# Kernel tuning notes

Measured on AMD Instinct MI355X. Metric: run time of the kernel, lower is better.

## Reference

```python
import jax, jax.numpy as jnp
import numpy as np

B, S, D = 2, 2048, 2048
NH, NKV, HD = 16, 4, 128
REP = NH // NKV
EPS = 1e-6
ROPE_THETA = 1e6


def setup_inputs() -> dict:
    key = jax.random.key(0)
    ks = jax.random.split(key, 6)
    x = jax.random.normal(ks[0], (B, S, D), jnp.float32)
    # real rotary embeddings: [S, HD]
    inv_freq = 1.0 / (ROPE_THETA ** (np.arange(0, HD, 2, dtype=np.float64) / HD))
    freqs = np.outer(np.arange(S, dtype=np.float64), inv_freq)
    emb = np.concatenate([freqs, freqs], axis=-1)
    cos = jnp.asarray(np.cos(emb), jnp.float32)
    sin = jnp.asarray(np.sin(emb), jnp.float32)
    scale = 1.0 / np.sqrt(D)
    Wq = jax.random.normal(ks[1], (D, NH * HD), jnp.float32) * scale   # [in, out]
    Wk = jax.random.normal(ks[2], (D, NKV * HD), jnp.float32) * scale
    Wv = jax.random.normal(ks[3], (D, NKV * HD), jnp.float32) * scale
    Wo = jax.random.normal(ks[4], (NH * HD, D), jnp.float32) * (1.0 / np.sqrt(NH * HD))
    q_norm_w = jnp.ones((HD,), jnp.float32)
    k_norm_w = jnp.ones((HD,), jnp.float32)
    return dict(x=x, cos=cos, sin=sin, Wq=Wq, Wk=Wk, Wv=Wv, Wo=Wo,
                q_norm_w=q_norm_w, k_norm_w=k_norm_w)


def _rms_norm(h, w):
    var = jnp.mean(h * h, axis=-1, keepdims=True)
    return w * (h * jax.lax.rsqrt(var + EPS))


def _rotate_half(h):
    h1, h2 = jnp.split(h, 2, axis=-1)
    return jnp.concatenate([-h2, h1], axis=-1)


def reference(x, cos, sin, Wq, Wk, Wv, Wo, q_norm_w, k_norm_w):
    b, s, _ = x.shape
    q = (x @ Wq).reshape(b, s, NH, HD)
    k = (x @ Wk).reshape(b, s, NKV, HD)
    v = (x @ Wv).reshape(b, s, NKV, HD)
    # per-head QK RMSNorm
    q = _rms_norm(q, q_norm_w)
    k = _rms_norm(k, k_norm_w)
    # RoPE: cos/sin [S,HD] -> broadcast over batch and heads
    c = cos[None, :, None, :]
    s_ = sin[None, :, None, :]
    q = q * c + _rotate_half(q) * s_
    k = k * c + _rotate_half(k) * s_
    # GQA: group q heads per kv head instead of materializing repeat_kv
    qg = q.reshape(b, s, NKV, REP, HD)
    scores = jnp.einsum('bqgrd,bkgd->bgrqk', qg, k) / np.sqrt(HD)
    causal = jnp.tril(jnp.ones((s, s), bool))  # [q,k]
    scores = jnp.where(causal, scores, -jnp.inf)
    probs = jax.nn.softmax(scores.astype(jnp.float32), axis=-1).astype(q.dtype)
    out = jnp.einsum('bgrqk,bkgd->bqgrd', probs, v).reshape(b, s, NH * HD)
    return out @ Wo
```

## Files before the change

kernel.cpp:

```cpp
#include <hip/hip_runtime.h>
#include <hip/hip_bf16.h>
#include <math.h>

#define B_ 2
#define S_ 2048
#define D_ 2048
#define NH_ 16
#define NKV_ 4
#define HD_ 128
#define EPS_ 1e-6f
#define SCALE_ 0.08838834764831845f
#define LOG2E_ 1.4426950408889634f
#define KOFF_ 2048
#define VOFF_ 2560
#define MINIT_ -1e30f

typedef float f32x4 __attribute__((ext_vector_type(4)));
typedef short bf16x8 __attribute__((ext_vector_type(8)));
typedef short short4v __attribute__((ext_vector_type(4)));
typedef float float4v __attribute__((ext_vector_type(4)));
typedef unsigned uint2v __attribute__((ext_vector_type(2)));
typedef unsigned uint4v __attribute__((ext_vector_type(4)));

static __device__ __forceinline__ short f2bf(float f) {
    union { float f; unsigned u; } x{f};
    unsigned r = (x.u + 0x7fff + ((x.u >> 16) & 1)) >> 16;
    return (short)r;
}
static __device__ __forceinline__ float bf2f(short s) {
    union { unsigned u; float f; } x; x.u = ((unsigned)(unsigned short)s) << 16; return x.f;
}
static __device__ __forceinline__ unsigned pack_bf2(float a, float b) {
    return __builtin_amdgcn_perm(__builtin_bit_cast(unsigned, b),
                                 __builtin_bit_cast(unsigned, a), 0x07060302u);
}

#define AS1(p) ((const __attribute__((address_space(1))) void*)(p))
#define AS3(p) ((__attribute__((address_space(3))) void*)(p))
static __device__ __forceinline__ void async16(const void* g, void* l) {
    __builtin_amdgcn_global_load_lds(AS1(g), AS3(l), 16, 0, 0);
}

__global__ __launch_bounds__(256) void cast_kernel(const float* __restrict__ in,
                                                   short* __restrict__ out) {
    size_t i = ((size_t)blockIdx.x * 256 + threadIdx.x) * 4;
    float4v v = *(const float4v*)(in + i);
    short4v o; o.x = f2bf(v.x); o.y = f2bf(v.y); o.z = f2bf(v.z); o.w = f2bf(v.w);
    *(short4v*)(out + i) = o;
}

__global__ __launch_bounds__(256) void transpose_all_kernel(const float* __restrict__ Wq,
                                                            const float* __restrict__ Wk,
                                                            const float* __restrict__ Wv,
                                                            const float* __restrict__ Wo,
                                                            short* __restrict__ Wt,
                                                            short* __restrict__ Wot) {
    __shared__ float tile[64][65];
    const int bx = blockIdx.x, by = blockIdx.y;
    const float* src; short* dst; int N, nb;
    if (bx < 32)      { src = Wq; dst = Wt;                         N = 2048; nb = bx; }
    else if (bx < 40) { src = Wk; dst = Wt + (size_t)KOFF_ * 2048;  N = 512;  nb = bx - 32; }
    else if (bx < 48) { src = Wv; dst = Wt + (size_t)VOFF_ * 2048;  N = 512;  nb = bx - 40; }
    else              { src = Wo; dst = Wot;                        N = 2048; nb = bx - 48; }
    const int n0 = nb * 64, k0 = by * 64;
    const int tid = threadIdx.x;
    for (int r = 0; r < 16; ++r) {
        int k = r * 4 + (tid >> 6);
        int n = tid & 63;
        tile[k][n] = src[(size_t)(k0 + k) * N + n0 + n];
    }
    __syncthreads();
    for (int r = 0; r < 4; ++r) {
        int n  = r * 16 + (tid >> 4);
        int kk = (tid & 15) * 4;
        short4v o4;
        o4.x = f2bf(tile[kk + 0][n]); o4.y = f2bf(tile[kk + 1][n]);
        o4.z = f2bf(tile[kk + 2][n]); o4.w = f2bf(tile[kk + 3][n]);
        *(short4v*)&dst[(size_t)(n0 + n) * 2048 + k0 + kk] = o4;
    }
}

__global__ __launch_bounds__(512, 2) void gemm_oproj_kernel(const short* __restrict__ A,
                                                            const short* __restrict__ Bt,
                                                            float* __restrict__ C) {
    __shared__ __align__(16) short smem[49152];
    short* A0 = smem;
    short* A1 = smem + 8192;
    short* B0 = smem + 16384;
    short* B1 = smem + 32768;

    const int tid  = threadIdx.x;
    const int orig = blockIdx.y * 8 + blockIdx.x;
    const int swz  = (orig & 7) * 32 + (orig >> 3);
    const int bn = swz & 7, bm = swz >> 3;
    const int wave = tid >> 6, lane = tid & 63;
    const int quad = lane >> 4, l16 = lane & 15;
    const int wr = wave >> 2, wc = wave & 3;

    const short* Ag = A  + (size_t)(bm * 128) * 2048;
    const short* Bg = Bt + (size_t)(bn * 256) * 2048;

    f32x4 acc[4][4];
#pragma unroll
    for (int i = 0; i < 4; ++i)
#pragma unroll
        for (int j = 0; j < 4; ++j) acc[i][j] = (f32x4){0.f, 0.f, 0.f, 0.f};

    bf16x8 a[4][2], b0[2][2], b1[2][2];

    auto stage_half = [&](const short* gpanel, int t, int h, short* lslot) {
#pragma unroll
        for (int u = 0; u < 2; ++u) {
            int ci = u * 512 + tid;
            int r  = ci >> 3;
            int cb = ((ci & 7) * 16) ^ ((r & 7) << 4);
            async16(gpanel + (size_t)(h * 128 + r) * 2048 + t * 64 + (cb >> 1),
                    lslot + h * 8192 + ci * 8);
        }
    };

#define OLDA_(lbuf) \
    _Pragma("unroll") for (int mt = 0; mt < 4; ++mt) \
    _Pragma("unroll") for (int ks = 0; ks < 2; ++ks) { \
        int row_ = wr * 64 + mt * 16 + l16; \
        int cb_  = (ks * 64 + quad * 16) ^ ((row_ & 7) << 4); \
        a[mt][ks] = *(const bf16x8*)&(lbuf)[row_ * 64 + (cb_ >> 1)]; \
    }
#define OLDB_(lbuf, qn, breg) \
    _Pragma("unroll") for (int ntl = 0; ntl < 2; ++ntl) \
    _Pragma("unroll") for (int ks = 0; ks < 2; ++ks) { \
        int row_ = wc * 64 + (qn) * 32 + ntl * 16 + l16; \
        int cb_  = (ks * 64 + quad * 16) ^ ((row_ & 7) << 4); \
        breg[ntl][ks] = *(const bf16x8*)&(lbuf)[row_ * 64 + (cb_ >> 1)]; \
    }
#define OBAR_() __builtin_amdgcn_s_barrier()
#define OMFMA_(qn, breg) do { \
    __builtin_amdgcn_s_setprio(1); \
    _Pragma("unroll") for (int mt = 0; mt < 4; ++mt) \
    _Pragma("unroll") for (int ntl = 0; ntl < 2; ++ntl) \
    _Pragma("unroll") for (int ks = 0; ks < 2; ++ks) \
        acc[mt][(qn) * 2 + ntl] = __builtin_amdgcn_mfma_f32_16x16x32_bf16( \
            a[mt][ks], breg[ntl][ks], acc[mt][(qn) * 2 + ntl], 0, 0, 0); \
    __builtin_amdgcn_s_setprio(0); __builtin_amdgcn_s_barrier(); } while (0)

    stage_half(Bg, 0, 0, B0); stage_half(Bg, 0, 1, B0);
    stage_half(Ag, 0, 0, A0);
    asm volatile("s_waitcnt vmcnt(0)" ::: "memory");
    __builtin_amdgcn_s_barrier();

#pragma unroll 1
    for (int i = 0; i < 16; ++i) {
        const int tE = 2 * i, tO = 2 * i + 1;
        const bool more = (i < 15);

        stage_half(Ag, tO, 0, A1);
        stage_half(Bg, tO, 0, B1); stage_half(Bg, tO, 1, B1);
        OLDA_(A0); OLDB_(B0, 0, b0);
        OBAR_();
        OMFMA_(0, b0);

        if (more) {
            stage_half(Ag, tE + 2, 0, A0);
            asm volatile("s_waitcnt vmcnt(2)" ::: "memory");
        } else {
            asm volatile("s_waitcnt vmcnt(0)" ::: "memory");
        }
        OLDB_(B0, 1, b1);
        OBAR_();
        OMFMA_(1, b1);

        if (more) { stage_half(Bg, tE + 2, 0, B0); stage_half(Bg, tE + 2, 1, B0); }
        OLDA_(A1); OLDB_(B1, 0, b0);
        OBAR_();
        OMFMA_(0, b0);

        if (more) { asm volatile("s_waitcnt vmcnt(0)" ::: "memory"); }
        OLDB_(B1, 1, b1);
        OBAR_();
        OMFMA_(1, b1);
    }

#pragma unroll
    for (int mt = 0; mt < 4; ++mt)
#pragma unroll
        for (int nt = 0; nt < 4; ++nt)
#pragma unroll
            for (int j = 0; j < 4; ++j) {
                int row = bm * 128 + wr * 64 + mt * 16 + quad * 4 + j;
                int col = bn * 256 + wc * 64 + nt * 16 + l16;
                C[(size_t)row * 2048 + col] = acc[mt][nt][j];
            }
#undef OLDA_
#undef OLDB_
#undef OBAR_
#undef OMFMA_
}

#define QKV_ITERS 16

__global__ __launch_bounds__(512, 2) void qkv_fused_kernel(const short* __restrict__ xb,
                                                           const short* __restrict__ Wt,
                                                           const float* __restrict__ cosb,
                                                           const float* __restrict__ sinb,
                                                           const float* __restrict__ qw,
                                                           const float* __restrict__ kw,
                                                           short* __restrict__ q_rope,
                                                           short* __restrict__ k_rope,
                                                           short* __restrict__ vtr) {
    __shared__ __align__(16) short smem[65536];
    __shared__ float ss2[4][256];

    short* A0 = smem;
    short* A1 = smem + 16384;
    short* B0 = smem + 32768;
    short* B1 = smem + 49152;

    const int tid  = threadIdx.x;
    const int orig = blockIdx.y * 12 + blockIdx.x;
    const int swz  = (orig & 7) * 24 + (orig >> 3);
    const int bn = swz % 12, bm = swz / 12;
    const int wave = tid >> 6, lane = tid & 63;
    const int quad = lane >> 4, l16 = lane & 15;
    const int wr = wave >> 2, wc = wave & 3;

    const short* Ag = xb + (size_t)(bm * 256) * 2048;
    const short* Bg = Wt + (size_t)(bn * 256) * 2048;

    f32x4 acc[8][4];
#pragma unroll
    for (int i = 0; i < 8; ++i)
#pragma unroll
        for (int j = 0; j < 4; ++j) acc[i][j] = (f32x4){0.f, 0.f, 0.f, 0.f};

    bf16x8 a[4][2], b0[2][2], b1[2][2];

    auto stage_half = [&](const short* gpanel, int t, int h, short* lslot) {
#pragma unroll
        for (int u = 0; u < 2; ++u) {
            int ci = u * 512 + tid;
            int r  = ci >> 3;
            int cb = ((ci & 7) * 16) ^ ((r & 7) << 4);
            async16(gpanel + (size_t)(h * 128 + r) * 2048 + t * 64 + (cb >> 1),
                    lslot + h * 8192 + ci * 8);
        }
    };

#define LDA_(lbuf, qm) \
    _Pragma("unroll") for (int mt = 0; mt < 4; ++mt) \
    _Pragma("unroll") for (int ks = 0; ks < 2; ++ks) { \
        int row_ = wr * 128 + (qm) * 64 + mt * 16 + l16; \
        int cb_  = (ks * 64 + quad * 16) ^ ((row_ & 7) << 4); \
        a[mt][ks] = *(const bf16x8*)&(lbuf)[row_ * 64 + (cb_ >> 1)]; \
    }
#define LDB_(lbuf, qn, breg) \
    _Pragma("unroll") for (int ntl = 0; ntl < 2; ++ntl) \
    _Pragma("unroll") for (int ks = 0; ks < 2; ++ks) { \
        int row_ = wc * 64 + (qn) * 32 + ntl * 16 + l16; \
        int cb_  = (ks * 64 + quad * 16) ^ ((row_ & 7) << 4); \
        breg[ntl][ks] = *(const bf16x8*)&(lbuf)[row_ * 64 + (cb_ >> 1)]; \
    }
#define MFMA16_(qm, qn, breg) \
    _Pragma("unroll") for (int mt = 0; mt < 4; ++mt) \
    _Pragma("unroll") for (int ntl = 0; ntl < 2; ++ntl) \
    _Pragma("unroll") for (int ks = 0; ks < 2; ++ks) \
        acc[(qm) * 4 + mt][(qn) * 2 + ntl] = __builtin_amdgcn_mfma_f32_16x16x32_bf16( \
            a[mt][ks], breg[ntl][ks], acc[(qm) * 4 + mt][(qn) * 2 + ntl], 0, 0, 0);
#define PH_BAR() __builtin_amdgcn_s_barrier()
#define PH_MFMA2(qm) do { \
        __builtin_amdgcn_s_setprio(1); MFMA16_(qm, 0, b0); MFMA16_(qm, 1, b1); \
        __builtin_amdgcn_s_setprio(0); \
        __builtin_amdgcn_s_barrier(); } while (0)

    stage_half(Bg, 0, 0, B0); stage_half(Bg, 0, 1, B0);
    stage_half(Ag, 0, 0, A0); stage_half(Ag, 0, 1, A0);
    stage_half(Bg, 1, 0, B1); stage_half(Bg, 1, 1, B1);
    asm volatile("s_waitcnt vmcnt(4)" ::: "memory");
    __builtin_amdgcn_s_barrier();

#pragma unroll 1
    for (int i = 0; i < QKV_ITERS; ++i) {
        const int tE = 2 * i, tO = 2 * i + 1;
        const bool more = (i < QKV_ITERS - 1);

        LDA_(A0, 0); LDB_(B0, 0, b0); LDB_(B0, 1, b1);
        stage_half(Ag, tO, 0, A1); stage_half(Ag, tO, 1, A1);
        PH_BAR();
        PH_MFMA2(0);

        LDA_(A0, 1);
        if (more) {
            stage_half(Bg, tE + 2, 0, B0); stage_half(Bg, tE + 2, 1, B0);
            asm volatile("s_waitcnt vmcnt(4)" ::: "memory");
        } else {
            asm volatile("s_waitcnt vmcnt(0)" ::: "memory");
        }
        PH_BAR();
        PH_MFMA2(1);

        LDA_(A1, 0); LDB_(B1, 0, b0); LDB_(B1, 1, b1);
        if (more) { stage_half(Ag, tE + 2, 0, A0); stage_half(Ag, tE + 2, 1, A0); }
        PH_BAR();
        PH_MFMA2(0);

        LDA_(A1, 1);
        if (more) {
            stage_half(Bg, tO + 2, 0, B1); stage_half(Bg, tO + 2, 1, B1);
            asm volatile("s_waitcnt vmcnt(4)" ::: "memory");
        }
        PH_BAR();
        PH_MFMA2(1);
    }

    if (bn >= 10) {
        const int gbase = (bn - 10) * 2;
#pragma unroll
        for (int am = 0; am < 8; ++am) {
            int tok0 = bm * 256 + wr * 128 + am * 16 + quad * 4;
            int bb = tok0 >> 11, s0 = tok0 & (S_ - 1);
#pragma unroll
            for (int nt = 0; nt < 4; ++nt) {
                int col = wc * 64 + nt * 16 + l16;
                int g = gbase + (col >> 7);
                int d = col & 127;
                short4v o4;
                o4.x = f2bf(acc[am][nt][0]); o4.y = f2bf(acc[am][nt][1]);
                o4.z = f2bf(acc[am][nt][2]); o4.w = f2bf(acc[am][nt][3]);
                *(short4v*)&vtr[((size_t)(bb * NKV_ + g) * HD_ + d) * S_ + s0] = o4;
            }
        }
        return;
    }

    {
        float pss[8][4];
#pragma unroll
        for (int am = 0; am < 8; ++am)
#pragma unroll
            for (int j = 0; j < 4; ++j) {
                float s = 0.f;
#pragma unroll
                for (int nt = 0; nt < 4; ++nt) s += acc[am][nt][j] * acc[am][nt][j];
                pss[am][j] = s;
            }
#pragma unroll
        for (int off = 1; off < 16; off <<= 1)
#pragma unroll
            for (int am = 0; am < 8; ++am)
#pragma unroll
                for (int j = 0; j < 4; ++j)
                    pss[am][j] += __shfl_xor(pss[am][j], off);
        if (l16 == 0)
#pragma unroll
            for (int am = 0; am < 8; ++am)
#pragma unroll
                for (int j = 0; j < 4; ++j)
                    ss2[wc][wr * 128 + am * 16 + quad * 4 + j] = pss[am][j];
    }
    short* ct = smem;
#pragma unroll
    for (int am = 0; am < 8; ++am)
#pragma unroll
        for (int nt = 0; nt < 4; ++nt)
#pragma unroll
            for (int j = 0; j < 4; ++j)
                ct[(wr * 128 + am * 16 + quad * 4 + j) * 256 + wc * 64 + nt * 16 + l16]
                    = f2bf(acc[am][nt][j]);
    __syncthreads();

    const bool isQ = (bn < 8);
    const float osc = isQ ? (SCALE_ * LOG2E_) : 1.0f;
    const float* w = isQ ? qw : kw;
#pragma unroll 1
    for (int it = 0; it < 16; ++it) {
        int idx = it * 512 + tid;
        int row = idx >> 5;
        int s32 = idx & 31;
        int head = s32 >> 4, seg = s32 & 15;
        int tok = bm * 256 + row;
        int bb = tok >> 11, s = tok & (S_ - 1);
        float rstd = rsqrtf((ss2[2 * head][row] + ss2[2 * head + 1][row]) * (1.0f / HD_) + EPS_);
        int c0 = seg * 8, p0 = (seg ^ 8) * 8;
        bf16x8 ta = *(const bf16x8*)&ct[row * 256 + head * 128 + c0];
        bf16x8 tb = *(const bf16x8*)&ct[row * 256 + head * 128 + p0];
        float sgn = (seg < 8) ? -1.0f : 1.0f;
        float4v cs0 = *(const float4v*)&cosb[(size_t)s * HD_ + c0];
        float4v cs1 = *(const float4v*)&cosb[(size_t)s * HD_ + c0 + 4];
        float4v sn0 = *(const float4v*)&sinb[(size_t)s * HD_ + c0];
        float4v sn1 = *(const float4v*)&sinb[(size_t)s * HD_ + c0 + 4];
        float ov[8];
#pragma unroll
        for (int i = 0; i < 8; ++i) {
            float n1 = bf2f(ta[i]) * rstd * w[c0 + i];
            float n2 = bf2f(tb[i]) * rstd * w[p0 + i];
            float cs = (i < 4) ? cs0[i & 3] : cs1[i & 3];
            float sn = (i < 4) ? sn0[i & 3] : sn1[i & 3];
            ov[i] = (n1 * cs + sgn * n2 * sn) * osc;
        }
        uint4v wv;
#pragma unroll
        for (int i2 = 0; i2 < 4; ++i2)
            wv[i2] = ((unsigned)(unsigned short)f2bf(ov[2 * i2])) |
                     ((unsigned)(unsigned short)f2bf(ov[2 * i2 + 1]) << 16);
        int gh = isQ ? (bn * 2 + head) : ((bn - 8) * 2 + head);
        short* dst = isQ
            ? q_rope + ((size_t)(bb * S_ + s) * NH_ + gh) * HD_ + c0
            : k_rope + ((size_t)(bb * NKV_ + gh) * S_ + s) * HD_ + c0;
        *(uint4v*)dst = wv;
    }
#undef LDA_
#undef LDB_
#undef MFMA16_
#undef PH_BAR
#undef PH_MFMA2
}

__global__ __launch_bounds__(512, 1) void attn_kernel(const short* __restrict__ qr,
                                                      const short* __restrict__ kg,
                                                      const short* __restrict__ vt,
                                                      short* __restrict__ aout) {
    __shared__ __align__(16) short Ks[2][2][8192];
    __shared__ __align__(16) short Vs[2][2][8192];

    const int lin = blockIdx.x;
    const int b  = lin & 1;
    const int g  = (lin >> 1) & 3;
    const int hq = (lin >> 3) & 3;
    const int pr = lin >> 5;
    const int h  = g * 4 + hq;

    const int wave = threadIdx.x >> 6, lane = threadIdx.x & 63;
    const int quad = lane >> 4, l16 = lane & 15;
    const int half = wave >> 2;
    const int ww   = wave & 3;

    const short* kbase = kg + (size_t)(b * NKV_ + g) * S_ * HD_;
    const short* vbase = vt + (size_t)(b * NKV_ + g) * HD_ * S_;

    auto stage = [&](int kt, short* Kd, short* Vd) {
        const short* kt_base = kbase + (size_t)kt * 64 * HD_;
        const short* vt_base = vbase + kt * 64;
#pragma unroll
        for (int t = 0; t < 2; ++t) {
            int ci  = (wave * 2 + t) * 64 + lane;
            int key = ci >> 4;
            int c   = (ci & 15) ^ ((key ^ (key >> 2)) & 15);
            async16(kt_base + key * HD_ + c * 8, Kd + ci * 8);
        }
#pragma unroll
        for (int t = 0; t < 2; ++t) {
            int ci = (wave * 2 + t) * 64 + lane;
            int d  = ci >> 3;
            int c  = (ci & 7) ^ (d & 7);
            async16(vt_base + (size_t)d * S_ + c * 8, Vd + ci * 8);
        }
    };

#pragma unroll 1
    for (int ph = 0; ph < 2; ++ph) {
        const int qt    = ph ? (15 - pr) : pr;
        const int nhalf = qt + 1;
        const int qrow0 = qt * 128 + ww * 16 + l16;
        const int qrow1 = qrow0 + 64;

        bf16x8 qf[2][4];
#pragma unroll
        for (int qs = 0; qs < 2; ++qs) {
            const short* qp = qr + ((size_t)(b * S_ + (qs ? qrow1 : qrow0)) * NH_ + h) * HD_;
#pragma unroll
            for (int ks = 0; ks < 4; ++ks)
                qf[qs][ks] = *(const bf16x8*)(qp + ks * 32 + quad * 8);
        }

        f32x4 o[2][8];
#pragma unroll
        for (int qs = 0; qs < 2; ++qs)
#pragma unroll
            for (int i = 0; i < 8; ++i) o[qs][i] = (f32x4){0.f, 0.f, 0.f, 0.f};
        float m_i[2] = {MINIT_, MINIT_};
        float l_i[2] = {0.f, 0.f};

        stage(0, Ks[0][0], Vs[0][0]);
        stage(1, Ks[1][0], Vs[1][0]);
        int buf = 0;
#pragma unroll 1
        for (int i = 0; i < nhalf; ++i) {
            __syncthreads();
            if (i + 1 < nhalf) {
                stage(2 * i + 2, Ks[0][buf ^ 1], Vs[0][buf ^ 1]);
                stage(2 * i + 3, Ks[1][buf ^ 1], Vs[1][buf ^ 1]);
            }
            const short* Kb = Ks[half][buf];
            const short* Vb = Vs[half][buf];
            const int ktm = 2 * i + half;

            f32x4 acc[2][4];
#pragma unroll
            for (int qs = 0; qs < 2; ++qs)
#pragma unroll
                for (int t = 0; t < 4; ++t) acc[qs][t] = (f32x4){0.f, 0.f, 0.f, 0.f};
            __builtin_amdgcn_s_setprio(1);
#pragma unroll
            for (int t = 0; t < 4; ++t) {
                int lk = ((t >> 1) << 5) + ((l16 >> 2) << 3) + ((t & 1) << 2) + (l16 & 3);
                const short* kp = &Kb[lk * 128];
                int pm = (lk ^ (lk >> 2)) & 15;
#pragma unroll
                for (int ks = 0; ks < 4; ++ks) {
                    bf16x8 kf = *(const bf16x8*)(kp + (((ks * 4 + quad) ^ pm) * 8));
                    acc[0][t] = __builtin_amdgcn_mfma_f32_16x16x32_bf16(kf, qf[0][ks], acc[0][t], 0, 0, 0);
                    acc[1][t] = __builtin_amdgcn_mfma_f32_16x16x32_bf16(kf, qf[1][ks], acc[1][t], 0, 0, 0);
                }
            }
            __builtin_amdgcn_s_setprio(0);
            const int key_base = ktm * 64;
#pragma unroll
            for (int qs = 0; qs < 2; ++qs) {
                int qmin = qt * 128 + qs * 64 + ww * 16;
                int qrow = qs ? qrow1 : qrow0;
                if (key_base + 63 > qmin) {
#pragma unroll
                    for (int t = 0; t < 4; ++t)
#pragma unroll
                        for (int j = 0; j < 4; ++j) {
                            int kl = key_base + ((t >> 1) << 5) + (quad << 3) + ((t & 1) << 2) + j;
                            if (kl > qrow) acc[qs][t][j] = -INFINITY;
                        }
                }
            }
            unsigned pk[2][2][4];
#pragma unroll
            for (int qs = 0; qs < 2; ++qs) {
                float mx = m_i[qs];
#pragma unroll
                for (int t = 0; t < 4; ++t)
#pragma unroll
                    for (int j = 0; j < 4; ++j) mx = fmaxf(mx, acc[qs][t][j]);
                mx = fmaxf(mx, __shfl_xor(mx, 16));
                mx = fmaxf(mx, __shfl_xor(mx, 32));
                float al = __builtin_amdgcn_exp2f(m_i[qs] - mx);
                m_i[qs] = mx;
                float rs = 0.f;
                float p[4][4];
#pragma unroll
                for (int t = 0; t < 4; ++t)
#pragma unroll
                    for (int j = 0; j < 4; ++j) {
                        float e = __builtin_amdgcn_exp2f(acc[qs][t][j] - mx);
                        p[t][j] = e;
                        rs += e;
                    }
                rs += __shfl_xor(rs, 16);
                rs += __shfl_xor(rs, 32);
                l_i[qs] = al * l_i[qs] + rs;
#pragma unroll
                for (int d8 = 0; d8 < 8; ++d8)
#pragma unroll
                    for (int j = 0; j < 4; ++j) o[qs][d8][j] *= al;
#pragma unroll
                for (int grp = 0; grp < 2; ++grp) {
                    pk[qs][grp][0] = pack_bf2(p[2 * grp][0],     p[2 * grp][1]);
                    pk[qs][grp][1] = pack_bf2(p[2 * grp][2],     p[2 * grp][3]);
                    pk[qs][grp][2] = pack_bf2(p[2 * grp + 1][0], p[2 * grp + 1][1]);
                    pk[qs][grp][3] = pack_bf2(p[2 * grp + 1][2], p[2 * grp + 1][3]);
                }
            }
            __builtin_amdgcn_s_setprio(1);
#pragma unroll
            for (int grp = 0; grp < 2; ++grp) {
                union { unsigned u[4]; bf16x8 v; } pb0, pb1;
#pragma unroll
                for (int i2 = 0; i2 < 4; ++i2) { pb0.u[i2] = pk[0][grp][i2]; pb1.u[i2] = pk[1][grp][i2]; }
#pragma unroll
                for (int d8 = 0; d8 < 8; ++d8) {
                    int d = d8 * 16 + l16;
                    bf16x8 vf = *(const bf16x8*)&Vb[d * 64 + (((grp * 4 + quad) ^ (d & 7)) * 8)];
                    o[0][d8] = __builtin_amdgcn_mfma_f32_16x16x32_bf16(vf, pb0.v, o[0][d8], 0, 0, 0);
                    o[1][d8] = __builtin_amdgcn_mfma_f32_16x16x32_bf16(vf, pb1.v, o[1][d8], 0, 0, 0);
                }
            }
            __builtin_amdgcn_s_setprio(0);
            buf ^= 1;
        }

        __syncthreads();
        float* exch = (float*)(ww < 2 ? &Ks[0][0][0] : &Vs[0][0][0]);
        float* slot = exch + ((size_t)((ww & 1) * 64 + lane) * 68);
        if (half == 1) {
#pragma unroll
            for (int qs = 0; qs < 2; ++qs) {
#pragma unroll
                for (int d8 = 0; d8 < 8; ++d8)
#pragma unroll
                    for (int j = 0; j < 4; ++j)
                        slot[qs * 32 + d8 * 4 + j] = o[qs][d8][j];
                slot[64 + qs] = m_i[qs];
                slot[66 + qs] = l_i[qs];
            }
        }
        __syncthreads();
        if (half == 0) {
#pragma unroll
            for (int qs = 0; qs < 2; ++qs) {
                float mB = slot[64 + qs], lB = slot[66 + qs];
                float m  = fmaxf(m_i[qs], mB);
                float wA = __builtin_amdgcn_exp2f(m_i[qs] - m);
                float wB = __builtin_amdgcn_exp2f(mB - m);
                float il = 1.0f / (l_i[qs] * wA + lB * wB);
                int qrow = qs ? qrow1 : qrow0;
                short* op = aout + ((size_t)(b * S_ + qrow) * NH_ + h) * HD_ + quad * 4;
#pragma unroll
                for (int d8 = 0; d8 < 8; ++d8) {
                    float v0 = (o[qs][d8][0] * wA + slot[qs * 32 + d8 * 4 + 0] * wB) * il;
                    float v1 = (o[qs][d8][1] * wA + slot[qs * 32 + d8 * 4 + 1] * wB) * il;
                    float v2 = (o[qs][d8][2] * wA + slot[qs * 32 + d8 * 4 + 2] * wB) * il;
                    float v3 = (o[qs][d8][3] * wA + slot[qs * 32 + d8 * 4 + 3] * wB) * il;
                    uint2v wv;
                    wv.x = ((unsigned)(unsigned short)f2bf(v0)) |
                           ((unsigned)(unsigned short)f2bf(v1) << 16);
                    wv.y = ((unsigned)(unsigned short)f2bf(v2)) |
                           ((unsigned)(unsigned short)f2bf(v3) << 16);
                    *(uint2v*)(op + d8 * 16) = wv;
                }
            }
        }
        __syncthreads();
    }
}

extern "C" void kernel_launch(void* const* d_in, const int* in_sizes, int n_in,
                              void* d_out, int out_size, void* d_ws, size_t ws_size,
                              hipStream_t stream) {
    (void)in_sizes; (void)n_in; (void)out_size; (void)ws_size;
    const float* x    = (const float*)d_in[0];
    const float* cosb = (const float*)d_in[1];
    const float* sinb = (const float*)d_in[2];
    const float* Wq   = (const float*)d_in[3];
    const float* Wk   = (const float*)d_in[4];
    const float* Wv   = (const float*)d_in[5];
    const float* Wo   = (const float*)d_in[6];
    const float* qw   = (const float*)d_in[7];
    const float* kw   = (const float*)d_in[8];
    float* out = (float*)d_out;

    char* ws = (char*)d_ws;
    short* xb     = (short*)ws;  ws += (size_t)4096 * 2048 * 2;
    short* Wt     = (short*)ws;  ws += (size_t)3072 * 2048 * 2;
    short* Wot    = (short*)ws;  ws += (size_t)2048 * 2048 * 2;
    short* q_rope = (short*)ws;  ws += (size_t)4096 * 2048 * 2;
    short* k_rope = (short*)ws;  ws += (size_t)4096 * 512 * 2;
    short* vt     = (short*)ws;  ws += (size_t)4096 * 512 * 2;
    short* a_out  = (short*)ws;  ws += (size_t)4096 * 2048 * 2;

    const int M = B_ * S_;

    cast_kernel<<<M * 2048 / 1024, 256, 0, stream>>>(x, xb);
    transpose_all_kernel<<<dim3(80, 32), 256, 0, stream>>>(Wq, Wk, Wv, Wo, Wt, Wot);

    qkv_fused_kernel<<<dim3(12, M / 256), 512, 0, stream>>>(
        xb, Wt, cosb, sinb, qw, kw, q_rope, k_rope, vt);

    attn_kernel<<<256, 512, 0, stream>>>(q_rope, k_rope, vt, a_out);

    gemm_oproj_kernel<<<dim3(8, 32), 512, 0, stream>>>(a_out, Wot, out);
}
```

Before: 287.6 us.

## Retile QKV GEMM to 128x384 blocks with head-aligned per-row norm+RoPE epilogue

Result: no change. 289.7 us (+0.7%).

```diff
diff --git a/kernel.cpp b/kernel.cpp
--- a/kernel.cpp
+++ b/kernel.cpp
@@ -40,6 +40,7 @@
 static __device__ __forceinline__ void async16(const void* g, void* l) {
     __builtin_amdgcn_global_load_lds(AS1(g), AS3(l), 16, 0, 0);
 }
+#define SB_() __builtin_amdgcn_sched_barrier(0)
 
 __global__ __launch_bounds__(256) void cast_kernel(const float* __restrict__ in,
                                                    short* __restrict__ out) {
@@ -208,31 +209,30 @@
                                                            short* __restrict__ k_rope,
                                                            short* __restrict__ vtr) {
     __shared__ __align__(16) short smem[65536];
-    __shared__ float ss2[4][256];
 
     short* A0 = smem;
-    short* A1 = smem + 16384;
-    short* B0 = smem + 32768;
-    short* B1 = smem + 49152;
+    short* A1 = smem + 8192;
+    short* B0 = smem + 16384;
+    short* B1 = smem + 40960;
 
     const int tid  = threadIdx.x;
-    const int orig = blockIdx.y * 12 + blockIdx.x;
-    const int swz  = (orig & 7) * 24 + (orig >> 3);
-    const int bn = swz % 12, bm = swz / 12;
+    const int orig = blockIdx.y * 8 + blockIdx.x;
+    const int swz  = (orig & 7) * 32 + (orig >> 3);
+    const int bn = swz >> 5, bm = swz & 31;
     const int wave = tid >> 6, lane = tid & 63;
     const int quad = lane >> 4, l16 = lane & 15;
     const int wr = wave >> 2, wc = wave & 3;
 
-    const short* Ag = xb + (size_t)(bm * 256) * 2048;
-    const short* Bg = Wt + (size_t)(bn * 256) * 2048;
-
-    f32x4 acc[8][4];
-#pragma unroll
-    for (int i = 0; i < 8; ++i)
-#pragma unroll
-        for (int j = 0; j < 4; ++j) acc[i][j] = (f32x4){0.f, 0.f, 0.f, 0.f};
-
-    bf16x8 a[4][2], b0[2][2], b1[2][2];
+    const short* Ag = xb + (size_t)(bm * 128) * 2048;
+    const short* Bg = Wt + (size_t)(bn * 384) * 2048;
+
+    f32x4 acc[4][6];
+#pragma unroll
+    for (int i = 0; i < 4; ++i)
+#pragma unroll
+        for (int j = 0; j < 6; ++j) acc[i][j] = (f32x4){0.f, 0.f, 0.f, 0.f};
+
+    bf16x8 a[4][2], b0[3][2], b1[3][2];
 
     auto stage_half = [&](const short* gpanel, int t, int h, short* lslot) {
 #pragma unroll
@@ -245,36 +245,35 @@
         }
     };
 
-#define LDA_(lbuf, qm) \
+#define LDA_(lbuf) \
     _Pragma("unroll") for (int mt = 0; mt < 4; ++mt) \
     _Pragma("unroll") for (int ks = 0; ks < 2; ++ks) { \
-        int row_ = wr * 128 + (qm) * 64 + mt * 16 + l16; \
+        int row_ = wr * 64 + mt * 16 + l16; \
         int cb_  = (ks * 64 + quad * 16) ^ ((row_ & 7) << 4); \
         a[mt][ks] = *(const bf16x8*)&(lbuf)[row_ * 64 + (cb_ >> 1)]; \
     }
 #define LDB_(lbuf, qn, breg) \
-    _Pragma("unroll") for (int ntl = 0; ntl < 2; ++ntl) \
+    _Pragma("unroll") for (int ntl = 0; ntl < 3; ++ntl) \
     _Pragma("unroll") for (int ks = 0; ks < 2; ++ks) { \
-        int row_ = wc * 64 + (qn) * 32 + ntl * 16 + l16; \
+        int row_ = wc * 96 + (qn) * 48 + ntl * 16 + l16; \
         int cb_  = (ks * 64 + quad * 16) ^ ((row_ & 7) << 4); \
         breg[ntl][ks] = *(const bf16x8*)&(lbuf)[row_ * 64 + (cb_ >> 1)]; \
     }
-#define MFMA16_(qm, qn, breg) \
-    _Pragma("unroll") for (int mt = 0; mt < 4; ++mt) \
-    _Pragma("unroll") for (int ntl = 0; ntl < 2; ++ntl) \
-    _Pragma("unroll") for (int ks = 0; ks < 2; ++ks) \
-        acc[(qm) * 4 + mt][(qn) * 2 + ntl] = __builtin_amdgcn_mfma_f32_16x16x32_bf16( \
-            a[mt][ks], breg[ntl][ks], acc[(qm) * 4 + mt][(qn) * 2 + ntl], 0, 0, 0);
-#define PH_BAR() __builtin_amdgcn_s_barrier()
-#define PH_MFMA2(qm) do { \
-        __builtin_amdgcn_s_setprio(1); MFMA16_(qm, 0, b0); MFMA16_(qm, 1, b1); \
+#define PH_BAR() do { __builtin_amdgcn_sched_barrier(0); __builtin_amdgcn_s_barrier(); } while (0)
+#define PH_MFMA24(qn, breg) do { \
+        __builtin_amdgcn_s_setprio(1); \
+        _Pragma("unroll") for (int mt = 0; mt < 4; ++mt) \
+        _Pragma("unroll") for (int ntl = 0; ntl < 3; ++ntl) \
+        _Pragma("unroll") for (int ks = 0; ks < 2; ++ks) \
+            acc[mt][(qn) * 3 + ntl] = __builtin_amdgcn_mfma_f32_16x16x32_bf16( \
+                a[mt][ks], breg[ntl][ks], acc[mt][(qn) * 3 + ntl], 0, 0, 0); \
         __builtin_amdgcn_s_setprio(0); \
-        __builtin_amdgcn_s_barrier(); } while (0)
-
-    stage_half(Bg, 0, 0, B0); stage_half(Bg, 0, 1, B0);
-    stage_half(Ag, 0, 0, A0); stage_half(Ag, 0, 1, A0);
-    stage_half(Bg, 1, 0, B1); stage_half(Bg, 1, 1, B1);
-    asm volatile("s_waitcnt vmcnt(4)" ::: "memory");
+        __builtin_amdgcn_sched_barrier(0); __builtin_amdgcn_s_barrier(); } while (0)
+
+    stage_half(Bg, 0, 0, B0); stage_half(Bg, 0, 1, B0); stage_half(Bg, 0, 2, B0);
+    stage_half(Ag, 0, 0, A0);
+    stage_half(Ag, 1, 0, A1);
+    asm volatile("s_waitcnt vmcnt(2)" ::: "memory");
     __builtin_amdgcn_s_barrier();
 
 #pragma unroll 1
@@ -282,136 +281,119 @@
         const int tE = 2 * i, tO = 2 * i + 1;
         const bool more = (i < QKV_ITERS - 1);
 
-        LDA_(A0, 0); LDB_(B0, 0, b0); LDB_(B0, 1, b1);
-        stage_half(Ag, tO, 0, A1); stage_half(Ag, tO, 1, A1);
+        LDA_(A0); LDB_(B0, 0, b0);
+        stage_half(Bg, tO, 0, B1); stage_half(Bg, tO, 1, B1); stage_half(Bg, tO, 2, B1);
         PH_BAR();
-        PH_MFMA2(0);
-
-        LDA_(A0, 1);
+        PH_MFMA24(0, b0);
+
+        LDB_(B0, 1, b1);
         if (more) {
-            stage_half(Bg, tE + 2, 0, B0); stage_half(Bg, tE + 2, 1, B0);
-            asm volatile("s_waitcnt vmcnt(4)" ::: "memory");
+            stage_half(Ag, tE + 2, 0, A0);
+            asm volatile("s_waitcnt vmcnt(2)" ::: "memory");
         } else {
             asm volatile("s_waitcnt vmcnt(0)" ::: "memory");
         }
         PH_BAR();
-        PH_MFMA2(1);
-
-        LDA_(A1, 0); LDB_(B1, 0, b0); LDB_(B1, 1, b1);
-        if (more) { stage_half(Ag, tE + 2, 0, A0); stage_half(Ag, tE + 2, 1, A0); }
+        PH_MFMA24(1, b1);
+
+        LDA_(A1); LDB_(B1, 0, b0);
+        if (more) { stage_half(Bg, tE + 2, 0, B0); stage_half(Bg, tE + 2, 1, B0); stage_half(Bg, tE + 2, 2, B0); }
         PH_BAR();
-        PH_MFMA2(0);
-
-        LDA_(A1, 1);
+        PH_MFMA24(0, b0);
+
+        LDB_(B1, 1, b1);
         if (more) {
-            stage_half(Bg, tO + 2, 0, B1); stage_half(Bg, tO + 2, 1, B1);
-            asm volatile("s_waitcnt vmcnt(4)" ::: "memory");
+            stage_half(Ag, tO + 2, 0, A1);
+            asm volatile("s_waitcnt vmcnt(2)" ::: "memory");
         }
         PH_BAR();
-        PH_MFMA2(1);
-    }
-
-    if (bn >= 10) {
-        const int gbase = (bn - 10) * 2;
-#pragma unroll
-        for (int am = 0; am < 8; ++am) {
-            int tok0 = bm * 256 + wr * 128 + am * 16 + quad * 4;
-            int bb = tok0 >> 11, s0 = tok0 & (S_ - 1);
-#pragma unroll
-            for (int nt = 0; nt < 4; ++nt) {
-                int col = wc * 64 + nt * 16 + l16;
-                int g = gbase + (col >> 7);
-                int d = col & 127;
+        PH_MFMA24(1, b1);
+    }
+
+#pragma unroll
+    for (int mt = 0; mt < 4; ++mt) {
+        int tok0 = bm * 128 + wr * 64 + mt * 16 + quad * 4;
+        int bb = tok0 >> 11, s0 = tok0 & (S_ - 1);
+#pragma unroll
+        for (int nt = 0; nt < 6; ++nt) {
+            int colh = wc * 96 + nt * 16;
+            int gh = bn * 3 + (colh >> 7);
+            if (gh >= 20) {
+                int g = gh - 20;
+                int d = (colh & 127) + l16;
                 short4v o4;
-                o4.x = f2bf(acc[am][nt][0]); o4.y = f2bf(acc[am][nt][1]);
-                o4.z = f2bf(acc[am][nt][2]); o4.w = f2bf(acc[am][nt][3]);
+                o4.x = f2bf(acc[mt][nt][0]); o4.y = f2bf(acc[mt][nt][1]);
+                o4.z = f2bf(acc[mt][nt][2]); o4.w = f2bf(acc[mt][nt][3]);
                 *(short4v*)&vtr[((size_t)(bb * NKV_ + g) * HD_ + d) * S_ + s0] = o4;
             }
         }
-        return;
-    }
-
-    {
-        float pss[8][4];
-#pragma unroll
-        for (int am = 0; am < 8; ++am)
-#pragma unroll
-            for (int j = 0; j < 4; ++j) {
-                float s = 0.f;
-#pragma unroll
-                for (int nt = 0; nt < 4; ++nt) s += acc[am][nt][j] * acc[am][nt][j];
-                pss[am][j] = s;
-            }
-#pragma unroll
-        for (int off = 1; off < 16; off <<= 1)
-#pragma unroll
-            for (int am = 0; am < 8; ++am)
-#pragma unroll
-                for (int j = 0; j < 4; ++j)
-                    pss[am][j] += __shfl_xor(pss[am][j], off);
-        if (l16 == 0)
-#pragma unroll
-            for (int am = 0; am < 8; ++am)
-#pragma unroll
-                for (int j = 0; j < 4; ++j)
-                    ss2[wc][wr * 128 + am * 16 + quad * 4 + j] = pss[am][j];
-    }
+    }
+    if (bn * 3 >= 20) return;
+
     short* ct = smem;
 #pragma unroll
-    for (int am = 0; am < 8; ++am)
-#pragma unroll
-        for (int nt = 0; nt < 4; ++nt)
+    for (int mt = 0; mt < 4; ++mt)
+#pragma unroll
+        for (int nt = 0; nt < 6; ++nt)
 #pragma unroll
             for (int j = 0; j < 4; ++j)
-                ct[(wr * 128 + am * 16 + quad * 4 + j) * 256 + wc * 64 + nt * 16 + l16]
-                    = f2bf(acc[am][nt][j]);
+                ct[(wr * 64 + mt * 16 + quad * 4 + j) * 386 + wc * 96 + nt * 16 + l16]
+                    = f2bf(acc[mt][nt][j]);
     __syncthreads();
 
-    const bool isQ = (bn < 8);
-    const float osc = isQ ? (SCALE_ * LOG2E_) : 1.0f;
-    const float* w = isQ ? qw : kw;
-#pragma unroll 1
-    for (int it = 0; it < 16; ++it) {
-        int idx = it * 512 + tid;
-        int row = idx >> 5;
-        int s32 = idx & 31;
-        int head = s32 >> 4, seg = s32 & 15;
-        int tok = bm * 256 + row;
-        int bb = tok >> 11, s = tok & (S_ - 1);
-        float rstd = rsqrtf((ss2[2 * head][row] + ss2[2 * head + 1][row]) * (1.0f / HD_) + EPS_);
-        int c0 = seg * 8, p0 = (seg ^ 8) * 8;
-        bf16x8 ta = *(const bf16x8*)&ct[row * 256 + head * 128 + c0];
-        bf16x8 tb = *(const bf16x8*)&ct[row * 256 + head * 128 + p0];
-        float sgn = (seg < 8) ? -1.0f : 1.0f;
-        float4v cs0 = *(const float4v*)&cosb[(size_t)s * HD_ + c0];
-        float4v cs1 = *(const float4v*)&cosb[(size_t)s * HD_ + c0 + 4];
-        float4v sn0 = *(const float4v*)&sinb[(size_t)s * HD_ + c0];
-        float4v sn1 = *(const float4v*)&sinb[(size_t)s * HD_ + c0 + 4];
-        float ov[8];
-#pragma unroll
-        for (int i = 0; i < 8; ++i) {
-            float n1 = bf2f(ta[i]) * rstd * w[c0 + i];
-            float n2 = bf2f(tb[i]) * rstd * w[p0 + i];
-            float cs = (i < 4) ? cs0[i & 3] : cs1[i & 3];
-            float sn = (i < 4) ? sn0[i & 3] : sn1[i & 3];
-            ov[i] = (n1 * cs + sgn * n2 * sn) * osc;
-        }
-        uint4v wv;
-#pragma unroll
-        for (int i2 = 0; i2 < 4; ++i2)
-            wv[i2] = ((unsigned)(unsigned short)f2bf(ov[2 * i2])) |
-                     ((unsigned)(unsigned short)f2bf(ov[2 * i2 + 1]) << 16);
-        int gh = isQ ? (bn * 2 + head) : ((bn - 8) * 2 + head);
-        short* dst = isQ
-            ? q_rope + ((size_t)(bb * S_ + s) * NH_ + gh) * HD_ + c0
-            : k_rope + ((size_t)(bb * NKV_ + gh) * S_ + s) * HD_ + c0;
-        *(uint4v*)dst = wv;
+    if (tid < 384) {
+        int hh = tid >> 7, row = tid & 127;
+        int gh = bn * 3 + hh;
+        if (gh < 20) {
+            const bool isQ = gh < 16;
+            const float osc = isQ ? (SCALE_ * LOG2E_) : 1.0f;
+            const float* w = isQ ? qw : kw;
+            const short* src = &ct[row * 386 + hh * 128];
+            bf16x8 rv[16];
+#pragma unroll
+            for (int i = 0; i < 16; ++i) rv[i] = *(const bf16x8*)(src + i * 8);
+            float ss = 0.f;
+#pragma unroll
+            for (int i = 0; i < 16; ++i)
+#pragma unroll
+                for (int j = 0; j < 8; ++j) { float f = bf2f(rv[i][j]); ss += f * f; }
+            float rstd = rsqrtf(ss * (1.0f / HD_) + EPS_);
+            int tok = bm * 128 + row;
+            int bb = tok >> 11, s = tok & (S_ - 1);
+            short* dst = isQ
+                ? q_rope + ((size_t)(bb * S_ + s) * NH_ + gh) * HD_
+                : k_rope + ((size_t)(bb * NKV_ + (gh - 16)) * S_ + s) * HD_;
+#pragma unroll
+            for (int sg = 0; sg < 16; ++sg) {
+                int c0 = sg * 8, p0 = (sg ^ 8) * 8;
+                bf16x8 ta = rv[sg], tb = rv[sg ^ 8];
+                float sgn = (sg < 8) ? -1.0f : 1.0f;
+                float4v cs0 = *(const float4v*)&cosb[(size_t)s * HD_ + c0];
+                float4v cs1 = *(const float4v*)&cosb[(size_t)s * HD_ + c0 + 4];
+                float4v sn0 = *(const float4v*)&sinb[(size_t)s * HD_ + c0];
+                float4v sn1 = *(const float4v*)&sinb[(size_t)s * HD_ + c0 + 4];
+                float ov[8];
+#pragma unroll
+                for (int i = 0; i < 8; ++i) {
+                    float n1 = bf2f(ta[i]) * rstd * w[c0 + i];
+                    float n2 = bf2f(tb[i]) * rstd * w[p0 + i];
+                    float cs = (i < 4) ? cs0[i & 3] : cs1[i & 3];
+                    float sn = (i < 4) ? sn0[i & 3] : sn1[i & 3];
+                    ov[i] = (n1 * cs + sgn * n2 * sn) * osc;
+                }
+                uint4v wv;
+#pragma unroll
+                for (int i2 = 0; i2 < 4; ++i2)
+                    wv[i2] = ((unsigned)(unsigned short)f2bf(ov[2 * i2])) |
+                             ((unsigned)(unsigned short)f2bf(ov[2 * i2 + 1]) << 16);
+                *(uint4v*)(dst + c0) = wv;
+            }
+        }
     }
 #undef LDA_
 #undef LDB_
-#undef MFMA16_
 #undef PH_BAR
-#undef PH_MFMA2
+#undef PH_MFMA24
 }
 
 __global__ __launch_bounds__(512, 1) void attn_kernel(const short* __restrict__ qr,
@@ -656,7 +638,7 @@
     cast_kernel<<<M * 2048 / 1024, 256, 0, stream>>>(x, xb);
     transpose_all_kernel<<<dim3(80, 32), 256, 0, stream>>>(Wq, Wk, Wv, Wo, Wt, Wot);
 
-    qkv_fused_kernel<<<dim3(12, M / 256), 512, 0, stream>>>(
+    qkv_fused_kernel<<<dim3(8, 32), 512, 0, stream>>>(
         xb, Wt, cosb, sinb, qw, kw, q_rope, k_rope, vt);
 
     attn_kernel<<<256, 512, 0, stream>>>(q_rope, k_rope, vt, a_out);
```
